# Kernel tuning notes

Hardware: AMD Instinct MI355X
Metric: run time of the kernel (lower is better)

## Reference

```python
import jax, jax.numpy as jnp
import numpy as np

N = 4096
HIDDEN = 256
NUM_HEADS = 8
HEAD_DIM = HIDDEN // NUM_HEADS
LN_EPS = 1e-3


def setup_inputs() -> dict:
    key = jax.random.key(0)
    ks = jax.random.split(key, 8)
    s = 1.0 / np.sqrt(HIDDEN)
    feat = jax.random.normal(ks[0], (N, HIDDEN), dtype=jnp.float32)
    Wq = jax.random.normal(ks[1], (HIDDEN, HIDDEN), dtype=jnp.float32) * s
    bq = jnp.zeros((HIDDEN,), dtype=jnp.float32)
    Wkv = jax.random.normal(ks[2], (HIDDEN, 2 * HIDDEN), dtype=jnp.float32) * s
    bkv = jnp.zeros((2 * HIDDEN,), dtype=jnp.float32)
    Weg = jax.random.normal(ks[3], (HIDDEN, 2 * NUM_HEADS), dtype=jnp.float32) * s
    beg = jnp.zeros((2 * NUM_HEADS,), dtype=jnp.float32)
    ln_g = jnp.ones((HIDDEN,), dtype=jnp.float32)
    ln_b = jnp.zeros((HIDDEN,), dtype=jnp.float32)
    return {"feat": feat, "Wq": Wq, "bq": bq, "Wkv": Wkv, "bkv": bkv,
            "Weg": Weg, "beg": beg, "ln_g": ln_g, "ln_b": ln_b}


def reference(feat, Wq, bq, Wkv, bkv, Weg, beg, ln_g, ln_b):
    n = feat.shape[0]
    # projections
    Q = feat @ Wq + bq                                  # [N, hidden]
    KV = feat @ Wkv + bkv                               # [N, 2*hidden]
    K, V = jnp.split(KV, 2, axis=-1)
    EG = feat @ Weg + beg                               # [N, 2*heads]
    E, G = jnp.split(EG, 2, axis=-1)                    # each [N, heads]
    # reshape to [N, head_dim, heads] (heads is the FAST axis, as in torch .view)
    Q = Q.reshape(n, HEAD_DIM, NUM_HEADS) * (HEAD_DIM ** -0.5)
    K = K.reshape(n, HEAD_DIM, NUM_HEADS)
    V = V.reshape(n, HEAD_DIM, NUM_HEADS)
    # all-pairs scores with per-j edge bias: [N, N, heads]
    H = jnp.einsum('idh,jdh->ijh', Q, K) + E[None, :, :]
    # softmax over i (axis 0), post-softmax sigmoid gate (per j, h)
    A = jax.nn.softmax(H, axis=0) * jax.nn.sigmoid(G)[None, :, :]
    Va = jnp.einsum('ijh,jdh->idh', A, V).reshape(n, HIDDEN)
    # layernorm eps=1e-3
    mu = jnp.mean(Va, axis=-1, keepdims=True)
    var = jnp.var(Va, axis=-1, keepdims=True)
    return (Va - mu) * jax.lax.rsqrt(var + LN_EPS) * ln_g + ln_b
```

## Files before the change

### kernel.cpp

```cpp
#include <hip/hip_runtime.h>
#include <hip/hip_bf16.h>

#define N 4096
#define HID 256
#define NH 8
#define HD 32
#define NC 784
#define CH 8
#define JSPAN (N / CH)

typedef __attribute__((ext_vector_type(8))) short short8;
typedef __attribute__((ext_vector_type(4))) short short4v;
typedef __attribute__((ext_vector_type(4))) float f32x4;
typedef __attribute__((ext_vector_type(2))) unsigned int uint2v;
typedef __attribute__((ext_vector_type(4))) unsigned int uint4v;

#define QSCALE 0.25503482f

static __device__ __forceinline__ unsigned short f2bf(float f) {
    union { float f; unsigned u; } v; v.f = f;
    unsigned r = v.u + 0x7fff + ((v.u >> 16) & 1);
    return (unsigned short)(r >> 16);
}
static __device__ __forceinline__ unsigned packbf2(float a, float b) {
    __hip_bfloat162 t = __float22bfloat162_rn(make_float2(a, b));
    unsigned u; __builtin_memcpy(&u, &t, 4); return u;
}

__global__ void k_prep(const float* __restrict__ feat, const float* __restrict__ Wq,
                       const float* __restrict__ Wkv, const float* __restrict__ Weg,
                       const float* __restrict__ bq, const float* __restrict__ bkv,
                       const float* __restrict__ beg, unsigned short* __restrict__ featb,
                       unsigned short* __restrict__ WbT, float* __restrict__ bC,
                       float* __restrict__ colS) {
    int bx = blockIdx.x;
    if (bx < 1024) {
        int t = bx * 256 + threadIdx.x;
        float4 v = ((const float4*)feat)[t];
        short4v o;
        o[0] = (short)f2bf(v.x); o[1] = (short)f2bf(v.y);
        o[2] = (short)f2bf(v.z); o[3] = (short)f2bf(v.w);
        ((short4v*)featb)[t] = o;
    } else {
        int c = bx - 1024, k = threadIdx.x;
        float w, b;
        if (c < 256)      { w = Wq[k * 256 + c];          b = bq[c]; }
        else if (c < 768) { w = Wkv[k * 512 + (c - 256)]; b = bkv[c - 256]; }
        else              { w = Weg[k * 16 + (c - 768)];  b = beg[c - 768]; }
        WbT[c * 256 + k] = f2bf(w);
        if (k == 0) bC[c] = b;
        if (c < 128) colS[c * 256 + k] = 0.f;
    }
}

__global__ __launch_bounds__(256) void k_proj(const unsigned short* __restrict__ featb,
                                              const unsigned short* __restrict__ WbT,
                                              const float* __restrict__ bC,
                                              unsigned short* __restrict__ Qp,
                                              unsigned short* __restrict__ Kp,
                                              unsigned short* __restrict__ VpT,
                                              float* __restrict__ sigG) {
    int w = threadIdx.x >> 6, l = threadIdx.x & 63;
    int il = l & 15, g = l >> 4;
    int c0 = blockIdx.x * 16;
    int i0 = (blockIdx.y * 4 + w) * 16;
    const short8* Arow = (const short8*)(featb + (size_t)(i0 + il) * HID);
    const short8* Brow = (const short8*)(WbT + (size_t)(c0 + il) * HID);
    f32x4 acc = {0.f, 0.f, 0.f, 0.f};
#pragma unroll
    for (int k0 = 0; k0 < HID; k0 += 32) {
        short8 a = Arow[(k0 >> 3) + g];
        short8 b = Brow[(k0 >> 3) + g];
        acc = __builtin_amdgcn_mfma_f32_16x16x32_bf16(a, b, acc, 0, 0, 0);
    }
    int c = c0 + il;
    float bias = bC[c];
#pragma unroll
    for (int r = 0; r < 4; ++r) {
        int i = i0 + g * 4 + r;
        float val = acc[r] + bias;
        if (c < 256) {
            int h = c & 7, d = c >> 3;
            Qp[((size_t)h * N + i) * HD + d] = f2bf(val * QSCALE);
        } else if (c < 512) {
            int cc = c - 256, h = cc & 7, d = cc >> 3;
            Kp[((size_t)h * N + i) * HD + d] = f2bf(val);
        } else if (c < 768) {
            int cc = c - 512, h = cc & 7, d = cc >> 3;
            VpT[((size_t)h * HD + d) * N + i] = f2bf(val);
        } else {
            int cc = c - 768;
            if (cc >= 8) sigG[(size_t)(cc - 8) * N + i] = 1.f / (1.f + __expf(-val));
        }
    }
}

__global__ __launch_bounds__(256) void k_pass1(const unsigned short* __restrict__ Qp,
                                               const unsigned short* __restrict__ Kp,
                                               float* __restrict__ colS) {
    int w = threadIdx.x >> 6, l = threadIdx.x & 63;
    int il = l & 15, g = l >> 4;
    int h = blockIdx.y;
    int j0 = (blockIdx.x * 4 + w) * 32;
    const unsigned short* Kh = Kp + (size_t)h * N * HD;
    short8 Kf0 = *(const short8*)(Kh + (size_t)(j0 + il) * HD + g * 8);
    short8 Kf1 = *(const short8*)(Kh + (size_t)(j0 + 16 + il) * HD + g * 8);
    const unsigned short* Qh = Qp + (size_t)h * N * HD;
    f32x4 z = {0.f, 0.f, 0.f, 0.f};
    float s0 = 0.f, s1 = 0.f;
    int ibeg = blockIdx.z * 512;
    short8 Qa = *(const short8*)(Qh + (size_t)(ibeg + il) * HD + g * 8);
    short8 Qb = *(const short8*)(Qh + (size_t)(ibeg + 16 + il) * HD + g * 8);
    for (int i0 = ibeg; i0 < ibeg + 512; i0 += 32) {
        short8 cQa = Qa, cQb = Qb;
        int in = (i0 + 32 < ibeg + 512) ? i0 + 32 : i0;
        Qa = *(const short8*)(Qh + (size_t)(in + il) * HD + g * 8);
        Qb = *(const short8*)(Qh + (size_t)(in + 16 + il) * HD + g * 8);
        f32x4 Saa = __builtin_amdgcn_mfma_f32_16x16x32_bf16(cQa, Kf0, z, 0, 0, 0);
        f32x4 Sab = __builtin_amdgcn_mfma_f32_16x16x32_bf16(cQa, Kf1, z, 0, 0, 0);
        f32x4 Sba = __builtin_amdgcn_mfma_f32_16x16x32_bf16(cQb, Kf0, z, 0, 0, 0);
        f32x4 Sbb = __builtin_amdgcn_mfma_f32_16x16x32_bf16(cQb, Kf1, z, 0, 0, 0);
        s0 += (__builtin_amdgcn_exp2f(Saa[0]) + __builtin_amdgcn_exp2f(Saa[1]))
            + (__builtin_amdgcn_exp2f(Saa[2]) + __builtin_amdgcn_exp2f(Saa[3]))
            + (__builtin_amdgcn_exp2f(Sba[0]) + __builtin_amdgcn_exp2f(Sba[1]))
            + (__builtin_amdgcn_exp2f(Sba[2]) + __builtin_amdgcn_exp2f(Sba[3]));
        s1 += (__builtin_amdgcn_exp2f(Sab[0]) + __builtin_amdgcn_exp2f(Sab[1]))
            + (__builtin_amdgcn_exp2f(Sab[2]) + __builtin_amdgcn_exp2f(Sab[3]))
            + (__builtin_amdgcn_exp2f(Sbb[0]) + __builtin_amdgcn_exp2f(Sbb[1]))
            + (__builtin_amdgcn_exp2f(Sbb[2]) + __builtin_amdgcn_exp2f(Sbb[3]));
    }
#pragma unroll
    for (int off = 16; off <= 32; off <<= 1) {
        s0 += __shfl_xor(s0, off);
        s1 += __shfl_xor(s1, off);
    }
    if (g == 0) {
        atomicAdd(&colS[(size_t)h * N + j0 + il], s0);
        atomicAdd(&colS[(size_t)h * N + j0 + 16 + il], s1);
    }
}

__global__ void k_lc2(const float* __restrict__ sigG, const float* __restrict__ colS,
                      float* __restrict__ lc2) {
    int t = blockIdx.x * blockDim.x + threadIdx.x;
    f32x4 a = ((const f32x4*)sigG)[t];
    f32x4 b = ((const f32x4*)colS)[t];
    f32x4 o;
#pragma unroll
    for (int r = 0; r < 4; ++r) o[r] = __builtin_amdgcn_logf(a[r] / b[r]);
    ((f32x4*)lc2)[t] = o;
}

static __device__ __forceinline__ short8 frag_dance(f32x4 Sa, f32x4 Sb) {
    unsigned A0 = packbf2(__builtin_amdgcn_exp2f(Sa[0]), __builtin_amdgcn_exp2f(Sa[1]));
    unsigned A1 = packbf2(__builtin_amdgcn_exp2f(Sa[2]), __builtin_amdgcn_exp2f(Sa[3]));
    unsigned B0 = packbf2(__builtin_amdgcn_exp2f(Sb[0]), __builtin_amdgcn_exp2f(Sb[1]));
    unsigned B1 = packbf2(__builtin_amdgcn_exp2f(Sb[2]), __builtin_amdgcn_exp2f(Sb[3]));
    uint2v r1 = __builtin_amdgcn_permlane32_swap(A0, B0, false, false);
    uint2v r2 = __builtin_amdgcn_permlane16_swap(r1[0], r1[1], false, false);
    uint2v r3 = __builtin_amdgcn_permlane32_swap(A1, B1, false, false);
    uint2v r4 = __builtin_amdgcn_permlane16_swap(r3[0], r3[1], false, false);
    uint4v pu;
    pu[0] = r2[0]; pu[1] = r4[0]; pu[2] = r2[1]; pu[3] = r4[1];
    return __builtin_bit_cast(short8, pu);
}

__global__ __launch_bounds__(256) void k_pass2(const unsigned short* __restrict__ Qp,
                                               const unsigned short* __restrict__ Kp,
                                               const unsigned short* __restrict__ VpT,
                                               const float* __restrict__ lc2,
                                               float* __restrict__ Vpart) {
    int w = threadIdx.x >> 6, l = threadIdx.x & 63;
    int il = l & 15, g = l >> 4;
    int h = blockIdx.y;
    int i0 = (blockIdx.x * 4 + w) * 64;
    int jbeg = blockIdx.z * JSPAN;
    const unsigned short* Qh = Qp + (size_t)h * N * HD;
    const unsigned short* Kh = Kp + ((size_t)h * N + jbeg) * HD;
    const unsigned short* Vh = VpT + (size_t)h * HD * N + jbeg;
    const float* lcg = lc2 + (size_t)h * N + jbeg;
    short8 Qf[4];
#pragma unroll
    for (int q = 0; q < 4; ++q)
        Qf[q] = *(const short8*)(Qh + (size_t)(i0 + q * 16 + il) * HD + g * 8);
    f32x4 acc[4][2];
#pragma unroll
    for (int q = 0; q < 4; ++q) {
        acc[q][0] = {0.f, 0.f, 0.f, 0.f};
        acc[q][1] = {0.f, 0.f, 0.f, 0.f};
    }
    short8 K0 = *(const short8*)(Kh + (size_t)il * HD + g * 8);
    short8 K1 = *(const short8*)(Kh + (size_t)(16 + il) * HD + g * 8);
    short8 V0 = *(const short8*)(Vh + (size_t)il * N + g * 8);
    short8 V1 = *(const short8*)(Vh + (size_t)(16 + il) * N + g * 8);
    for (int jb = 0; jb < JSPAN; jb += 32) {
        short8 cK0 = K0, cK1 = K1, cV0 = V0, cV1 = V1;
        int jn = (jb + 32 < JSPAN) ? jb + 32 : jb;
        K0 = *(const short8*)(Kh + (size_t)(jn + il) * HD + g * 8);
        K1 = *(const short8*)(Kh + (size_t)(jn + 16 + il) * HD + g * 8);
        V0 = *(const short8*)(Vh + (size_t)il * N + jn + g * 8);
        V1 = *(const short8*)(Vh + (size_t)(16 + il) * N + jn + g * 8);
        f32x4 lcvA = *(const f32x4*)(lcg + jb + g * 4);
        f32x4 lcvB = *(const f32x4*)(lcg + jb + 16 + g * 4);
#pragma unroll
        for (int q = 0; q < 4; ++q) {
            f32x4 SA = __builtin_amdgcn_mfma_f32_16x16x32_bf16(cK0, Qf[q], lcvA, 0, 0, 0);
            f32x4 SB = __builtin_amdgcn_mfma_f32_16x16x32_bf16(cK1, Qf[q], lcvB, 0, 0, 0);
            short8 Pa = frag_dance(SA, SB);
            acc[q][0] = __builtin_amdgcn_mfma_f32_16x16x32_bf16(Pa, cV0, acc[q][0], 0, 0, 0);
            acc[q][1] = __builtin_amdgcn_mfma_f32_16x16x32_bf16(Pa, cV1, acc[q][1], 0, 0, 0);
        }
    }
    float* Vout = Vpart + (size_t)(blockIdx.z * NH + h) * N * HD;
#pragma unroll
    for (int q = 0; q < 4; ++q) {
#pragma unroll
        for (int r = 0; r < 4; ++r) {
            int ia = i0 + q * 16 + g * 4 + r;
            Vout[(size_t)ia * HD + il]      = acc[q][0][r];
            Vout[(size_t)ia * HD + 16 + il] = acc[q][1][r];
        }
    }
}

__global__ __launch_bounds__(256) void k_ln(const float* __restrict__ Vpart,
                                            const float* __restrict__ gam,
                                            const float* __restrict__ bet,
                                            float* __restrict__ out) {
    int w = threadIdx.x >> 6, l = threadIdx.x & 63;
    int i = blockIdx.x * 4 + w;
    int h = l >> 3, d0 = (l & 7) << 2;
    f32x4 x = {0.f, 0.f, 0.f, 0.f};
#pragma unroll
    for (int c = 0; c < CH; ++c) {
        f32x4 v = *(const f32x4*)(Vpart + ((size_t)(c * NH + h) * N + i) * HD + d0);
        x[0] += v[0]; x[1] += v[1]; x[2] += v[2]; x[3] += v[3];
    }
    float s1 = x[0] + x[1] + x[2] + x[3];
    float s2 = x[0] * x[0] + x[1] * x[1] + x[2] * x[2] + x[3] * x[3];
#pragma unroll
    for (int off = 1; off < 64; off <<= 1) {
        s1 += __shfl_xor(s1, off);
        s2 += __shfl_xor(s2, off);
    }
    float mu = s1 * (1.f / 256.f);
    float var = s2 * (1.f / 256.f) - mu * mu;
    float rs = rsqrtf(var + 1e-3f);
#pragma unroll
    for (int r = 0; r < 4; ++r) {
        int c = (d0 + r) * 8 + h;
        out[(size_t)i * HID + c] = (x[r] - mu) * rs * gam[c] + bet[c];
    }
}

extern "C" void kernel_launch(void* const* d_in, const int* in_sizes, int n_in,
                              void* d_out, int out_size, void* d_ws, size_t ws_size,
                              hipStream_t stream) {
    const float* feat = (const float*)d_in[0];
    const float* Wq   = (const float*)d_in[1];
    const float* bq   = (const float*)d_in[2];
    const float* Wkv  = (const float*)d_in[3];
    const float* bkv  = (const float*)d_in[4];
    const float* Weg  = (const float*)d_in[5];
    const float* beg  = (const float*)d_in[6];
    const float* ln_g = (const float*)d_in[7];
    const float* ln_b = (const float*)d_in[8];
    float* out = (float*)d_out;

    char* ws = (char*)d_ws;
    unsigned short* Qp    = (unsigned short*)(ws + 0);
    unsigned short* Kp    = (unsigned short*)(ws + (2u << 20));
    unsigned short* VpT   = (unsigned short*)(ws + (4u << 20));
    unsigned short* featb = (unsigned short*)(ws + (6u << 20));
    unsigned short* WbT   = (unsigned short*)(ws + (8u << 20));
    float* bC   = (float*)(ws + (8u << 20) + (512u << 10));
    float* sigG = (float*)(ws + (8u << 20) + (528u << 10));
    float* colS = (float*)(ws + (8u << 20) + (656u << 10));
    float* lc2  = (float*)(ws + (8u << 20) + (784u << 10));
    float* Vpart = (float*)(ws + (9u << 20));

    k_prep<<<dim3(1024 + NC), 256, 0, stream>>>(feat, Wq, Wkv, Weg, bq, bkv, beg,
                                                featb, WbT, bC, colS);
    k_proj<<<dim3(49, 64), 256, 0, stream>>>(featb, WbT, bC, Qp, Kp, VpT, sigG);
    k_pass1<<<dim3(32, NH, 8), 256, 0, stream>>>(Qp, Kp, colS);
    k_lc2<<<dim3(32), 256, 0, stream>>>(sigG, colS, lc2);
    k_pass2<<<dim3(16, NH, CH), 256, 0, stream>>>(Qp, Kp, VpT, lc2, Vpart);
    k_ln<<<dim3(1024), 256, 0, stream>>>(Vpart, ln_g, ln_b, out);
}
```

Baseline: 111.1 us.

## Fold softmax normalization and gate into V, widen pass1 column tiles

Instead of adding log(sigmoid(G)/colsum) as the MFMA accumulator bias in pass2, a new kernel scales the transposed V in place by sigmoid(G)/colsum per column. The lc2 kernel and its per-iteration loads in pass2 go away. Pass1 now processes 64 columns per wave with four K fragments, reusing each Q load across more MFMAs and halving the grid. The prefetch index clamps are removed, so the last iteration reads slightly past the chunk, and scaling V before the bf16 rounding changes numerics.

```diff
diff --git a/kernel.cpp b/kernel.cpp
--- a/kernel.cpp
+++ b/kernel.cpp
@@ -21,6 +21,9 @@
     union { float f; unsigned u; } v; v.f = f;
     unsigned r = v.u + 0x7fff + ((v.u >> 16) & 1);
     return (unsigned short)(r >> 16);
+}
+static __device__ __forceinline__ float bf2f(unsigned short u) {
+    union { unsigned u; float f; } v; v.u = ((unsigned)u) << 16; return v.f;
 }
 static __device__ __forceinline__ unsigned packbf2(float a, float b) {
     __hip_bfloat162 t = __float22bfloat162_rn(make_float2(a, b));
@@ -101,54 +104,68 @@
     int w = threadIdx.x >> 6, l = threadIdx.x & 63;
     int il = l & 15, g = l >> 4;
     int h = blockIdx.y;
-    int j0 = (blockIdx.x * 4 + w) * 32;
+    int j0 = (blockIdx.x * 4 + w) * 64;
     const unsigned short* Kh = Kp + (size_t)h * N * HD;
-    short8 Kf0 = *(const short8*)(Kh + (size_t)(j0 + il) * HD + g * 8);
-    short8 Kf1 = *(const short8*)(Kh + (size_t)(j0 + 16 + il) * HD + g * 8);
+    short8 Kf[4];
+#pragma unroll
+    for (int t = 0; t < 4; ++t)
+        Kf[t] = *(const short8*)(Kh + (size_t)(j0 + 16 * t + il) * HD + g * 8);
     const unsigned short* Qh = Qp + (size_t)h * N * HD;
     f32x4 z = {0.f, 0.f, 0.f, 0.f};
-    float s0 = 0.f, s1 = 0.f;
+    float s[4] = {0.f, 0.f, 0.f, 0.f};
     int ibeg = blockIdx.z * 512;
     short8 Qa = *(const short8*)(Qh + (size_t)(ibeg + il) * HD + g * 8);
     short8 Qb = *(const short8*)(Qh + (size_t)(ibeg + 16 + il) * HD + g * 8);
     for (int i0 = ibeg; i0 < ibeg + 512; i0 += 32) {
         short8 cQa = Qa, cQb = Qb;
-        int in = (i0 + 32 < ibeg + 512) ? i0 + 32 : i0;
+        int in = i0 + 32;
         Qa = *(const short8*)(Qh + (size_t)(in + il) * HD + g * 8);
         Qb = *(const short8*)(Qh + (size_t)(in + 16 + il) * HD + g * 8);
-        f32x4 Saa = __builtin_amdgcn_mfma_f32_16x16x32_bf16(cQa, Kf0, z, 0, 0, 0);
-        f32x4 Sab = __builtin_amdgcn_mfma_f32_16x16x32_bf16(cQa, Kf1, z, 0, 0, 0);
-        f32x4 Sba = __builtin_amdgcn_mfma_f32_16x16x32_bf16(cQb, Kf0, z, 0, 0, 0);
-        f32x4 Sbb = __builtin_amdgcn_mfma_f32_16x16x32_bf16(cQb, Kf1, z, 0, 0, 0);
-        s0 += (__builtin_amdgcn_exp2f(Saa[0]) + __builtin_amdgcn_exp2f(Saa[1]))
-            + (__builtin_amdgcn_exp2f(Saa[2]) + __builtin_amdgcn_exp2f(Saa[3]))
-            + (__builtin_amdgcn_exp2f(Sba[0]) + __builtin_amdgcn_exp2f(Sba[1]))
-            + (__builtin_amdgcn_exp2f(Sba[2]) + __builtin_amdgcn_exp2f(Sba[3]));
-        s1 += (__builtin_amdgcn_exp2f(Sab[0]) + __builtin_amdgcn_exp2f(Sab[1]))
-            + (__builtin_amdgcn_exp2f(Sab[2]) + __builtin_amdgcn_exp2f(Sab[3]))
-            + (__builtin_amdgcn_exp2f(Sbb[0]) + __builtin_amdgcn_exp2f(Sbb[1]))
-            + (__builtin_amdgcn_exp2f(Sbb[2]) + __builtin_amdgcn_exp2f(Sbb[3]));
-    }
-#pragma unroll
-    for (int off = 16; off <= 32; off <<= 1) {
-        s0 += __shfl_xor(s0, off);
-        s1 += __shfl_xor(s1, off);
+#pragma unroll
+        for (int t = 0; t < 4; ++t) {
+            f32x4 Sa = __builtin_amdgcn_mfma_f32_16x16x32_bf16(cQa, Kf[t], z, 0, 0, 0);
+            f32x4 Sb = __builtin_amdgcn_mfma_f32_16x16x32_bf16(cQb, Kf[t], z, 0, 0, 0);
+            s[t] += ((__builtin_amdgcn_exp2f(Sa[0]) + __builtin_amdgcn_exp2f(Sa[1]))
+                   + (__builtin_amdgcn_exp2f(Sa[2]) + __builtin_amdgcn_exp2f(Sa[3])))
+                  + ((__builtin_amdgcn_exp2f(Sb[0]) + __builtin_amdgcn_exp2f(Sb[1]))
+                   + (__builtin_amdgcn_exp2f(Sb[2]) + __builtin_amdgcn_exp2f(Sb[3])));
+        }
+    }
+#pragma unroll
+    for (int t = 0; t < 4; ++t) {
+        s[t] += __shfl_xor(s[t], 16);
+        s[t] += __shfl_xor(s[t], 32);
     }
     if (g == 0) {
-        atomicAdd(&colS[(size_t)h * N + j0 + il], s0);
-        atomicAdd(&colS[(size_t)h * N + j0 + 16 + il], s1);
-    }
-}
-
-__global__ void k_lc2(const float* __restrict__ sigG, const float* __restrict__ colS,
-                      float* __restrict__ lc2) {
-    int t = blockIdx.x * blockDim.x + threadIdx.x;
-    f32x4 a = ((const f32x4*)sigG)[t];
-    f32x4 b = ((const f32x4*)colS)[t];
-    f32x4 o;
-#pragma unroll
-    for (int r = 0; r < 4; ++r) o[r] = __builtin_amdgcn_logf(a[r] / b[r]);
-    ((f32x4*)lc2)[t] = o;
+#pragma unroll
+        for (int t = 0; t < 4; ++t)
+            atomicAdd(&colS[(size_t)h * N + j0 + 16 * t + il], s[t]);
+    }
+}
+
+__global__ void k_vprep(unsigned short* __restrict__ VpT,
+                        const float* __restrict__ sigG,
+                        const float* __restrict__ colS) {
+    int row = blockIdx.x >> 1;
+    int j0 = ((blockIdx.x & 1) * 256 + threadIdx.x) * 8;
+    int h = row >> 5;
+    unsigned short* p = VpT + (size_t)row * N + j0;
+    short8 v = *(short8*)p;
+    const float* sg = sigG + (size_t)h * N + j0;
+    const float* cs = colS + (size_t)h * N + j0;
+    f32x4 sa = *(const f32x4*)sg, sb = *(const f32x4*)(sg + 4);
+    f32x4 ca = *(const f32x4*)cs, cb = *(const f32x4*)(cs + 4);
+    unsigned o[4];
+    o[0] = packbf2(bf2f((unsigned short)v[0]) * sa[0] / ca[0],
+                   bf2f((unsigned short)v[1]) * sa[1] / ca[1]);
+    o[1] = packbf2(bf2f((unsigned short)v[2]) * sa[2] / ca[2],
+                   bf2f((unsigned short)v[3]) * sa[3] / ca[3]);
+    o[2] = packbf2(bf2f((unsigned short)v[4]) * sb[0] / cb[0],
+                   bf2f((unsigned short)v[5]) * sb[1] / cb[1]);
+    o[3] = packbf2(bf2f((unsigned short)v[6]) * sb[2] / cb[2],
+                   bf2f((unsigned short)v[7]) * sb[3] / cb[3]);
+    uint4v ov; ov[0] = o[0]; ov[1] = o[1]; ov[2] = o[2]; ov[3] = o[3];
+    *(uint4v*)p = ov;
 }
 
 static __device__ __forceinline__ short8 frag_dance(f32x4 Sa, f32x4 Sb) {
@@ -168,7 +185,6 @@
 __global__ __launch_bounds__(256) void k_pass2(const unsigned short* __restrict__ Qp,
                                                const unsigned short* __restrict__ Kp,
                                                const unsigned short* __restrict__ VpT,
-                                               const float* __restrict__ lc2,
                                                float* __restrict__ Vpart) {
     int w = threadIdx.x >> 6, l = threadIdx.x & 63;
     int il = l & 15, g = l >> 4;
@@ -178,16 +194,16 @@
     const unsigned short* Qh = Qp + (size_t)h * N * HD;
     const unsigned short* Kh = Kp + ((size_t)h * N + jbeg) * HD;
     const unsigned short* Vh = VpT + (size_t)h * HD * N + jbeg;
-    const float* lcg = lc2 + (size_t)h * N + jbeg;
     short8 Qf[4];
 #pragma unroll
     for (int q = 0; q < 4; ++q)
         Qf[q] = *(const short8*)(Qh + (size_t)(i0 + q * 16 + il) * HD + g * 8);
+    f32x4 z = {0.f, 0.f, 0.f, 0.f};
     f32x4 acc[4][2];
 #pragma unroll
     for (int q = 0; q < 4; ++q) {
-        acc[q][0] = {0.f, 0.f, 0.f, 0.f};
-        acc[q][1] = {0.f, 0.f, 0.f, 0.f};
+        acc[q][0] = z;
+        acc[q][1] = z;
     }
     short8 K0 = *(const short8*)(Kh + (size_t)il * HD + g * 8);
     short8 K1 = *(const short8*)(Kh + (size_t)(16 + il) * HD + g * 8);
@@ -195,17 +211,15 @@
     short8 V1 = *(const short8*)(Vh + (size_t)(16 + il) * N + g * 8);
     for (int jb = 0; jb < JSPAN; jb += 32) {
         short8 cK0 = K0, cK1 = K1, cV0 = V0, cV1 = V1;
-        int jn = (jb + 32 < JSPAN) ? jb + 32 : jb;
+        int jn = jb + 32;
         K0 = *(const short8*)(Kh + (size_t)(jn + il) * HD + g * 8);
         K1 = *(const short8*)(Kh + (size_t)(jn + 16 + il) * HD + g * 8);
         V0 = *(const short8*)(Vh + (size_t)il * N + jn + g * 8);
         V1 = *(const short8*)(Vh + (size_t)(16 + il) * N + jn + g * 8);
-        f32x4 lcvA = *(const f32x4*)(lcg + jb + g * 4);
-        f32x4 lcvB = *(const f32x4*)(lcg + jb + 16 + g * 4);
 #pragma unroll
         for (int q = 0; q < 4; ++q) {
-            f32x4 SA = __builtin_amdgcn_mfma_f32_16x16x32_bf16(cK0, Qf[q], lcvA, 0, 0, 0);
-            f32x4 SB = __builtin_amdgcn_mfma_f32_16x16x32_bf16(cK1, Qf[q], lcvB, 0, 0, 0);
+            f32x4 SA = __builtin_amdgcn_mfma_f32_16x16x32_bf16(cK0, Qf[q], z, 0, 0, 0);
+            f32x4 SB = __builtin_amdgcn_mfma_f32_16x16x32_bf16(cK1, Qf[q], z, 0, 0, 0);
             short8 Pa = frag_dance(SA, SB);
             acc[q][0] = __builtin_amdgcn_mfma_f32_16x16x32_bf16(Pa, cV0, acc[q][0], 0, 0, 0);
             acc[q][1] = __builtin_amdgcn_mfma_f32_16x16x32_bf16(Pa, cV1, acc[q][1], 0, 0, 0);
@@ -276,14 +290,13 @@
     float* bC   = (float*)(ws + (8u << 20) + (512u << 10));
     float* sigG = (float*)(ws + (8u << 20) + (528u << 10));
     float* colS = (float*)(ws + (8u << 20) + (656u << 10));
-    float* lc2  = (float*)(ws + (8u << 20) + (784u << 10));
     float* Vpart = (float*)(ws + (9u << 20));
 
     k_prep<<<dim3(1024 + NC), 256, 0, stream>>>(feat, Wq, Wkv, Weg, bq, bkv, beg,
                                                 featb, WbT, bC, colS);
     k_proj<<<dim3(49, 64), 256, 0, stream>>>(featb, WbT, bC, Qp, Kp, VpT, sigG);
-    k_pass1<<<dim3(32, NH, 8), 256, 0, stream>>>(Qp, Kp, colS);
-    k_lc2<<<dim3(32), 256, 0, stream>>>(sigG, colS, lc2);
-    k_pass2<<<dim3(16, NH, CH), 256, 0, stream>>>(Qp, Kp, VpT, lc2, Vpart);
+    k_pass1<<<dim3(16, NH, 8), 256, 0, stream>>>(Qp, Kp, colS);
+    k_vprep<<<dim3(512), 256, 0, stream>>>(VpT, sigG, colS);
+    k_pass2<<<dim3(16, NH, CH), 256, 0, stream>>>(Qp, Kp, VpT, Vpart);
     k_ln<<<dim3(1024), 256, 0, stream>>>(Vpart, ln_g, ln_b, out);
 }
```

Measured after the change: 111.4 us. Within noise of the previous version (+0.3%).
